# Kernel optimization log

Hardware: AMD Instinct MI355X
Metric: run time of the kernel (lower is better)

Reference implementation:

```python
import jax, jax.numpy as jnp
import numpy as np

# dims (match init_kwargs)
N, M = 128, 2048
DX, DY, DU, DZ = 64, 8, 256, 256
EPS = 0.01


def setup_inputs() -> dict:
    key = jax.random.key(0)
    kit = iter(jax.random.split(key, 40))
    def w(*shape):
        fan_in = shape[-1]
        return jax.random.normal(next(kit), shape, jnp.float32) / np.float32(np.sqrt(fan_in))
    def b(*shape):
        return 0.1 * jax.random.normal(next(kit), shape, jnp.float32)
    inp = {
        'X_tensor': jax.random.normal(next(kit), (N, DX), jnp.float32),
        'U_tensor': jax.random.normal(next(kit), (M, DY), jnp.float32),
        'Y_tensor': jax.random.normal(next(kit), (N, DY), jnp.float32),
        # context path (x -> u_i)
        'Wt0': w(DU, DX), 'bt0': b(DU),
        'Wt1': w(DU, DU), 'bt1': b(DU),
        # PICNN cell 0 (input cell, no z term)
        'Wyu0': w(DY, DX), 'byu0': b(DY), 'Wy0': w(DZ, DY), 'Wu0': w(DZ, DX), 'b0': b(DZ),
        # PICNN cell 1 (hidden cell, nonneg Wz1 via softplus)
        'Wzu1': w(DZ, DU), 'bzu1': b(DZ), 'Wz1': w(DZ, DZ),
        'Wyu1': w(DY, DU), 'byu1': b(DY), 'Wy1': w(DZ, DY), 'Wu1': w(DZ, DU), 'b1': b(DZ),
        # PICNN cell 2 (output cell, scalar potential)
        'Wzu2': w(DZ, DU), 'bzu2': b(DZ), 'Wz2': w(1, DZ),
        'Wyu2': w(DY, DU), 'byu2': b(DY), 'Wy2': w(1, DY), 'Wu2': w(1, DU), 'b2': b(1),
    }
    return inp


def _psi(X, U, Y, Wt0, bt0, Wt1, bt1, Wyu0, byu0, Wy0, Wu0, b0,
         Wzu1, bzu1, Wz1, Wyu1, byu1, Wy1, Wu1, b1,
         Wzu2, bzu2, Wz2, Wyu2, byu2, Wy2, Wu2, b2):
    relu = jax.nn.relu
    # context path depends only on X -> compute once per row, broadcast over m samples
    u1 = relu(X @ Wt0.T + bt0)                       # [n, du]
    u2 = relu(u1 @ Wt1.T + bt1)                      # [n, du]
    # cell 0: z1 [n, m, dz]  (pairwise over X rows x U samples)
    gy0 = X @ Wyu0.T + byu0                          # [n, dy]
    z1 = relu(jnp.einsum('md,nd,zd->nmz', U, gy0, Wy0)
              + (X @ Wu0.T + b0)[:, None, :])
    # cell 1: hidden convex cell with nonneg z-weight
    gz1 = relu(u1 @ Wzu1.T + bzu1)                   # [n, dz]
    gy1 = u1 @ Wyu1.T + byu1                         # [n, dy]
    z2 = relu(jnp.einsum('nmz,nz,kz->nmk', z1, gz1, jax.nn.softplus(Wz1))
              + jnp.einsum('md,nd,kd->nmk', U, gy1, Wy1)
              + (u1 @ Wu1.T + b1)[:, None, :])       # [n, m, dz]
    # output cell -> scalar potential phi(x_i, u_j)
    gz2 = relu(u2 @ Wzu2.T + bzu2)                   # [n, dz]
    gy2 = u2 @ Wyu2.T + byu2                         # [n, dy]
    phi = (jnp.einsum('nmz,nz,z->nm', z2, gz2, jax.nn.softplus(Wz2)[0])
           + jnp.einsum('md,nd,d->nm', U, gy2, Wy2[0])
           + (u2 @ Wu2[0] + b2[0])[:, None])         # [n, m]
    # entropic OT dual psi with stable row-wise logsumexp
    cost = Y @ U.T                                   # [n, m]
    slack = cost - phi
    row_max = jnp.max(slack, axis=1, keepdims=True)
    log_mean_exp = (jax.nn.logsumexp((slack - row_max) / EPS, axis=1, keepdims=True)
                    - jnp.log(jnp.float32(slack.shape[1])))
    return EPS * (log_mean_exp + row_max / EPS)      # [n, 1]


def reference(X_tensor, U_tensor, Y_tensor, Wt0, bt0, Wt1, bt1, Wyu0, byu0, Wy0, Wu0, b0,
              Wzu1, bzu1, Wz1, Wyu1, byu1, Wy1, Wu1, b1,
              Wzu2, bzu2, Wz2, Wyu2, byu2, Wy2, Wu2, b2):
    return _psi(X_tensor, U_tensor, Y_tensor, Wt0, bt0, Wt1, bt1, Wyu0, byu0, Wy0, Wu0, b0,
                Wzu1, bzu1, Wz1, Wyu1, byu1, Wy1, Wu1, b1,
                Wzu2, bzu2, Wz2, Wyu2, byu2, Wy2, Wu2, b2)
```

## Files before the change

kernel.cpp:

```cpp
#include <hip/hip_runtime.h>

#define NN 128
#define MM 2048
#define EPSF 0.01f

typedef __bf16 bf16x8 __attribute__((ext_vector_type(8)));
typedef __bf16 bf16x4 __attribute__((ext_vector_type(4)));
typedef float  f32x4  __attribute__((ext_vector_type(4)));

#define WS_SLACK 0
#define WS_W2    262144
#define WS_GZ1   294912
#define WS_YV    327680
#define WS_CU2   328704
#define WS_WTF   328832
#define WS_A2    361600
#define WS_B2    394368
#define WS_BX    918656
#define WS_U1    1442944
#define WS_U2    1459328
#define WS_C0    1475712
#define WS_C1    1492096
#define WS_GY0   1508480
#define WS_GY1   1509504

__device__ __forceinline__ float softplusf(float x) {
    return x > 20.f ? x : log1pf(expf(x));
}

__device__ __forceinline__ bf16x8 ld_cvt8(const float* __restrict__ p) {
    const float4* p4 = (const float4*)p;
    float4 a = p4[0], b = p4[1];
    bf16x8 r;
    r[0] = (__bf16)a.x; r[1] = (__bf16)a.y; r[2] = (__bf16)a.z; r[3] = (__bf16)a.w;
    r[4] = (__bf16)b.x; r[5] = (__bf16)b.y; r[6] = (__bf16)b.z; r[7] = (__bf16)b.w;
    return r;
}

__global__ __launch_bounds__(256) void k_l1(
    const float* __restrict__ X,
    const float* __restrict__ Wt0, const float* __restrict__ bt0,
    const float* __restrict__ Wu0, const float* __restrict__ b0,
    const float* __restrict__ Wyu0, const float* __restrict__ byu0,
    float* __restrict__ ws)
{
    const int t = threadIdx.x, w = t >> 6, lane = t & 63;
    const int c = lane & 15, q = lane >> 4;
    const int nb = blockIdx.y * 16;
    const int ct = blockIdx.x * 4 + w;
    if (ct >= 33) return;

    bf16x8 a1[2];
#pragma unroll
    for (int ch = 0; ch < 2; ++ch)
        a1[ch] = ld_cvt8(X + (nb + c) * 64 + ch * 32 + q * 8);

    const float* rp;
    int col;
    if (ct < 16)      { col = ct * 16 + c;        rp = Wt0 + col * 64; }
    else if (ct < 32) { col = (ct - 16) * 16 + c; rp = Wu0 + col * 64; }
    else              { col = c & 7;              rp = Wyu0 + col * 64; }

    f32x4 D = {0.f, 0.f, 0.f, 0.f};
#pragma unroll
    for (int ch = 0; ch < 2; ++ch) {
        bf16x8 b = ld_cvt8(rp + ch * 32 + q * 8);
        D = __builtin_amdgcn_mfma_f32_16x16x32_bf16(a1[ch], b, D, 0, 0, 0);
    }

    if (ct < 16) {
        __bf16* u1p = (__bf16*)(ws + WS_U1);
        const float bv = bt0[col];
#pragma unroll
        for (int r = 0; r < 4; ++r)
            u1p[(nb + 4 * q + r) * 256 + col] = (__bf16)fmaxf(D[r] + bv, 0.f);
    } else if (ct < 32) {
        __bf16* c0p = (__bf16*)(ws + WS_C0);
        const float bv = b0[col];
#pragma unroll
        for (int r = 0; r < 4; ++r)
            c0p[(nb + 4 * q + r) * 256 + col] = (__bf16)(D[r] + bv);
    } else if (c < 8) {
        const float bv = byu0[c];
#pragma unroll
        for (int r = 0; r < 4; ++r)
            ws[WS_GY0 + (nb + 4 * q + r) * 8 + c] = D[r] + bv;
    }
}

__global__ __launch_bounds__(256) void k_l2(
    const float* __restrict__ Wt1, const float* __restrict__ bt1,
    const float* __restrict__ Wzu1, const float* __restrict__ bzu1,
    const float* __restrict__ Wu1, const float* __restrict__ b1,
    const float* __restrict__ Wyu1, const float* __restrict__ byu1,
    float* __restrict__ ws)
{
    const int t = threadIdx.x, w = t >> 6, lane = t & 63;
    const int c = lane & 15, q = lane >> 4;
    const int nb = blockIdx.y * 16;
    const int ct = blockIdx.x * 4 + w;
    if (ct >= 49) return;

    const __bf16* u1p = (const __bf16*)(ws + WS_U1);
    bf16x8 aF[8];
#pragma unroll
    for (int ch = 0; ch < 8; ++ch)
        aF[ch] = *(const bf16x8*)(u1p + (nb + c) * 256 + ch * 32 + q * 8);

    const float* rp;
    int col;
    if (ct < 16)      { col = ct * 16 + c;        rp = Wt1 + col * 256; }
    else if (ct < 32) { col = (ct - 16) * 16 + c; rp = Wzu1 + col * 256; }
    else if (ct < 48) { col = (ct - 32) * 16 + c; rp = Wu1 + col * 256; }
    else              { col = c & 7;              rp = Wyu1 + col * 256; }

    f32x4 D = {0.f, 0.f, 0.f, 0.f};
#pragma unroll
    for (int ch = 0; ch < 8; ++ch) {
        bf16x8 b = ld_cvt8(rp + ch * 32 + q * 8);
        D = __builtin_amdgcn_mfma_f32_16x16x32_bf16(aF[ch], b, D, 0, 0, 0);
    }

    if (ct < 16) {
        __bf16* u2p = (__bf16*)(ws + WS_U2);
        const float bv = bt1[col];
#pragma unroll
        for (int r = 0; r < 4; ++r)
            u2p[(nb + 4 * q + r) * 256 + col] = (__bf16)fmaxf(D[r] + bv, 0.f);
    } else if (ct < 32) {
        const float bv = bzu1[col];
#pragma unroll
        for (int r = 0; r < 4; ++r)
            ws[WS_GZ1 + (nb + 4 * q + r) * 256 + col] = fmaxf(D[r] + bv, 0.f);
    } else if (ct < 48) {
        __bf16* c1p = (__bf16*)(ws + WS_C1);
        const float bv = b1[col];
#pragma unroll
        for (int r = 0; r < 4; ++r)
            c1p[(nb + 4 * q + r) * 256 + col] = (__bf16)(D[r] + bv);
    } else if (c < 8) {
        const float bv = byu1[c];
#pragma unroll
        for (int r = 0; r < 4; ++r)
            ws[WS_GY1 + (nb + 4 * q + r) * 8 + c] = D[r] + bv;
    }
}

__global__ __launch_bounds__(256) void k_l3(
    const float* __restrict__ Y,
    const float* __restrict__ Wzu2, const float* __restrict__ bzu2,
    const float* __restrict__ Wz2,
    const float* __restrict__ Wyu2, const float* __restrict__ byu2,
    const float* __restrict__ Wy2,
    const float* __restrict__ Wu2, const float* __restrict__ b2,
    float* __restrict__ ws)
{
    const int t = threadIdx.x, w = t >> 6, lane = t & 63;
    const int c = lane & 15, q = lane >> 4;
    const int nb = blockIdx.y * 16;
    const int ct = blockIdx.x * 4 + w;
    if (ct >= 17) return;

    const __bf16* u2p = (const __bf16*)(ws + WS_U2);
    bf16x8 aF[8];
#pragma unroll
    for (int ch = 0; ch < 8; ++ch)
        aF[ch] = *(const bf16x8*)(u2p + (nb + c) * 256 + ch * 32 + q * 8);

    const float* rp;
    int col = 0;
    if (ct < 16) { col = ct * 16 + c; rp = Wzu2 + col * 256; }
    else         { rp = (c < 8) ? (Wyu2 + c * 256) : Wu2; }

    f32x4 D = {0.f, 0.f, 0.f, 0.f};
#pragma unroll
    for (int ch = 0; ch < 8; ++ch) {
        bf16x8 b = ld_cvt8(rp + ch * 32 + q * 8);
        D = __builtin_amdgcn_mfma_f32_16x16x32_bf16(aF[ch], b, D, 0, 0, 0);
    }

    if (ct < 16) {
        const float bv = bzu2[col];
        const float sp = softplusf(Wz2[col]);
#pragma unroll
        for (int r = 0; r < 4; ++r) {
            float gz2 = fmaxf(D[r] + bv, 0.f);
            ws[WS_W2 + (nb + 4 * q + r) * 256 + col] = gz2 * sp;
        }
    } else if (c < 8) {
        const float bv = byu2[c];
        const float wy2 = Wy2[c];
#pragma unroll
        for (int r = 0; r < 4; ++r) {
            const int n = nb + 4 * q + r;
            ws[WS_YV + n * 8 + c] = Y[n * 8 + c] - (D[r] + bv) * wy2;
        }
    } else if (c == 8) {
#pragma unroll
        for (int r = 0; r < 4; ++r)
            ws[WS_CU2 + nb + 4 * q + r] = D[r] + b2[0];
    }
}

__global__ __launch_bounds__(256) void k_bmat(
    const float* __restrict__ Wz1, const float* __restrict__ U,
    const float* __restrict__ Wy0, const float* __restrict__ Wy1,
    float* __restrict__ ws)
{
    const int b = blockIdx.x, t = threadIdx.x;
    const int i = b * 256 + t;

    if (b < 64) {
        const int o = i * 4;
        const int j0 = o & 7;
        const int c  = (o >> 3) & 15;
        const int q  = (o >> 7) & 3;
        const int ch = (o >> 9) & 7;
        const int kt = o >> 12;
        const float* src = Wz1 + (kt * 16 + c) * 256 + ch * 32 + q * 8 + j0;
        float4 v = *(const float4*)src;
        bf16x4 r;
        r[0] = (__bf16)softplusf(v.x); r[1] = (__bf16)softplusf(v.y);
        r[2] = (__bf16)softplusf(v.z); r[3] = (__bf16)softplusf(v.w);
        *(bf16x4*)((__bf16*)(ws + WS_WTF) + o) = r;
    }
    {
        int m = i >> 5, cc = i & 31;
        float v = cc < 8 ? U[m * 8 + cc] : (cc == 8 ? 1.f : 0.f);
        ((__bf16*)(ws + WS_A2))[i] = (__bf16)v;
    }

    const int which = b >> 7, n = b & 127, z = t;
    const float* wy = (which ? Wy1 : Wy0) + z * 8;
    const float* gy = ws + (which ? WS_GY1 : WS_GY0) + n * 8;
    const __bf16* cp = (const __bf16*)(ws + (which ? WS_C1 : WS_C0)) + n * 256 + z;
    __bf16* dst = (__bf16*)(ws + (which ? WS_BX : WS_B2)) + (n * 256 + z) * 32;

    bf16x8 zz;
#pragma unroll
    for (int j = 0; j < 8; ++j) zz[j] = (__bf16)0.f;
    bf16x8 v0, v1 = zz;
#pragma unroll
    for (int d = 0; d < 8; ++d) v0[d] = (__bf16)(gy[d] * wy[d]);
    v1[0] = *cp;
    *(bf16x8*)(dst)      = v0;
    *(bf16x8*)(dst + 8)  = v1;
    *(bf16x8*)(dst + 16) = zz;
    *(bf16x8*)(dst + 24) = zz;
}

__global__ __launch_bounds__(256, 4) void k_main(
    const float* __restrict__ U,
    float* __restrict__ ws)
{
    __shared__ __bf16 zh[64][264];
    __shared__ float gz1s[256];
    __shared__ float w2s[256];
    __shared__ float sdot[64];
    __shared__ float psum[4][64];

    const int t  = threadIdx.x;
    const int n  = blockIdx.y;
    const int m0 = blockIdx.x * 64;
    const int w    = t >> 6;
    const int lane = t & 63;
    const int c = lane & 15;
    const int q = lane >> 4;

    gz1s[t] = ws[WS_GZ1 + n * 256 + t];
    w2s[t]  = ws[WS_W2  + n * 256 + t];
    if (t < 64) {
        float sd = 0.f;
#pragma unroll
        for (int d = 0; d < 8; ++d)
            sd += U[(m0 + t) * 8 + d] * ws[WS_YV + n * 8 + d];
        sdot[t] = sd;
    }

    const __bf16* A2p = (const __bf16*)(ws + WS_A2);
    const __bf16* B2p = (const __bf16*)(ws + WS_B2) + n * 8192;
    const __bf16* BXp = (const __bf16*)(ws + WS_BX) + n * 8192;
    const __bf16* WTF = (const __bf16*)(ws + WS_WTF);

    bf16x8 a2f[4];
#pragma unroll
    for (int mi = 0; mi < 4; ++mi)
        a2f[mi] = *(const bf16x8*)(A2p + (m0 + 16 * mi + c) * 32 + q * 8);

    {
        bf16x8 b2f[4];
#pragma unroll
        for (int zt = 0; zt < 4; ++zt)
            b2f[zt] = *(const bf16x8*)(B2p + (64 * w + 16 * zt + c) * 32 + q * 8);
        f32x4 pre[4][4];
#pragma unroll
        for (int zt = 0; zt < 4; ++zt)
#pragma unroll
            for (int mi = 0; mi < 4; ++mi) {
                f32x4 zacc = {0.f, 0.f, 0.f, 0.f};
                pre[zt][mi] = __builtin_amdgcn_mfma_f32_16x16x32_bf16(
                    b2f[zt], a2f[mi], zacc, 0, 0, 0);
            }
#pragma unroll
        for (int zt = 0; zt < 4; ++zt) {
            const int zb = 64 * w + 16 * zt + 4 * q;
#pragma unroll
            for (int mi = 0; mi < 4; ++mi) {
                bf16x4 v4;
#pragma unroll
                for (int r = 0; r < 4; ++r)
                    v4[r] = (__bf16)(fmaxf(pre[zt][mi][r], 0.f) * gz1s[zb + r]);
                *(bf16x4*)&zh[c + 16 * mi][zb] = v4;
            }
        }
    }

    f32x4 acc[4][4];
#pragma unroll
    for (int mi = 0; mi < 4; ++mi)
#pragma unroll
        for (int kj = 0; kj < 4; ++kj)
            acc[mi][kj] = f32x4{0.f, 0.f, 0.f, 0.f};

    __syncthreads();

    for (int ch = 0; ch < 8; ++ch) {
        bf16x8 az[4], bw[4];
#pragma unroll
        for (int mi = 0; mi < 4; ++mi)
            az[mi] = *(const bf16x8*)&zh[c + 16 * mi][ch * 32 + q * 8];
#pragma unroll
        for (int kj = 0; kj < 4; ++kj)
            bw[kj] = *(const bf16x8*)(WTF + ((4 * w + kj) * 8 + ch) * 512 + lane * 8);
#pragma unroll
        for (int mi = 0; mi < 4; ++mi)
#pragma unroll
            for (int kj = 0; kj < 4; ++kj)
                acc[mi][kj] = __builtin_amdgcn_mfma_f32_16x16x32_bf16(
                    az[mi], bw[kj], acc[mi][kj], 0, 0, 0);
    }
    {
        bf16x8 bx[4];
#pragma unroll
        for (int kj = 0; kj < 4; ++kj)
            bx[kj] = *(const bf16x8*)(BXp + (64 * w + 16 * kj + c) * 32 + q * 8);
#pragma unroll
        for (int mi = 0; mi < 4; ++mi)
#pragma unroll
            for (int kj = 0; kj < 4; ++kj)
                acc[mi][kj] = __builtin_amdgcn_mfma_f32_16x16x32_bf16(
                    a2f[mi], bx[kj], acc[mi][kj], 0, 0, 0);
    }

    float p[4][4];
#pragma unroll
    for (int mi = 0; mi < 4; ++mi)
#pragma unroll
        for (int r = 0; r < 4; ++r) p[mi][r] = 0.f;
#pragma unroll
    for (int kj = 0; kj < 4; ++kj) {
        float w2v = w2s[64 * w + 16 * kj + c];
#pragma unroll
        for (int mi = 0; mi < 4; ++mi)
#pragma unroll
            for (int r = 0; r < 4; ++r)
                p[mi][r] += fmaxf(acc[mi][kj][r], 0.f) * w2v;
    }
#pragma unroll
    for (int mi = 0; mi < 4; ++mi)
#pragma unroll
        for (int r = 0; r < 4; ++r) {
            float v = p[mi][r];
            v += __shfl_xor(v, 8);
            v += __shfl_xor(v, 4);
            v += __shfl_xor(v, 2);
            v += __shfl_xor(v, 1);
            p[mi][r] = v;
        }
    if (c == 0) {
#pragma unroll
        for (int mi = 0; mi < 4; ++mi)
            *(float4*)&psum[w][16 * mi + 4 * q] =
                make_float4(p[mi][0], p[mi][1], p[mi][2], p[mi][3]);
    }
    __syncthreads();
    if (t < 64) {
        float cu2 = ws[WS_CU2 + n];
        float pp = psum[0][t] + psum[1][t] + psum[2][t] + psum[3][t];
        ws[WS_SLACK + n * 2048 + m0 + t] = sdot[t] - cu2 - pp;
    }
}

__global__ __launch_bounds__(256) void k_lse(const float* __restrict__ ws,
                                             float* __restrict__ out) {
    __shared__ float redmax[4];
    __shared__ float redsum[4];
    const int n = blockIdx.x;
    const int t = threadIdx.x;
    const float* s = ws + WS_SLACK + n * 2048;

    float vals[8];
    float mx = -3.4e38f;
#pragma unroll
    for (int i = 0; i < 8; ++i) {
        vals[i] = s[t + 256 * i];
        mx = fmaxf(mx, vals[i]);
    }
#pragma unroll
    for (int off = 32; off; off >>= 1) mx = fmaxf(mx, __shfl_xor(mx, off));
    if ((t & 63) == 0) redmax[t >> 6] = mx;
    __syncthreads();
    mx = fmaxf(fmaxf(redmax[0], redmax[1]), fmaxf(redmax[2], redmax[3]));

    float sum = 0.f;
#pragma unroll
    for (int i = 0; i < 8; ++i) sum += expf((vals[i] - mx) * (1.f / EPSF));
#pragma unroll
    for (int off = 32; off; off >>= 1) sum += __shfl_xor(sum, off);
    if ((t & 63) == 0) redsum[t >> 6] = sum;
    __syncthreads();
    if (t == 0) {
        float S = redsum[0] + redsum[1] + redsum[2] + redsum[3];
        out[n] = EPSF * logf(S * (1.f / 2048.f)) + mx;
    }
}

extern "C" void kernel_launch(void* const* d_in, const int* in_sizes, int n_in,
                              void* d_out, int out_size, void* d_ws, size_t ws_size,
                              hipStream_t stream) {
    const float* X    = (const float*)d_in[0];
    const float* Uu   = (const float*)d_in[1];
    const float* Yy   = (const float*)d_in[2];
    const float* Wt0  = (const float*)d_in[3];
    const float* bt0  = (const float*)d_in[4];
    const float* Wt1  = (const float*)d_in[5];
    const float* bt1  = (const float*)d_in[6];
    const float* Wyu0 = (const float*)d_in[7];
    const float* byu0 = (const float*)d_in[8];
    const float* Wy0  = (const float*)d_in[9];
    const float* Wu0  = (const float*)d_in[10];
    const float* b0   = (const float*)d_in[11];
    const float* Wzu1 = (const float*)d_in[12];
    const float* bzu1 = (const float*)d_in[13];
    const float* Wz1  = (const float*)d_in[14];
    const float* Wyu1 = (const float*)d_in[15];
    const float* byu1 = (const float*)d_in[16];
    const float* Wy1  = (const float*)d_in[17];
    const float* Wu1  = (const float*)d_in[18];
    const float* b1   = (const float*)d_in[19];
    const float* Wzu2 = (const float*)d_in[20];
    const float* bzu2 = (const float*)d_in[21];
    const float* Wz2  = (const float*)d_in[22];
    const float* Wyu2 = (const float*)d_in[23];
    const float* byu2 = (const float*)d_in[24];
    const float* Wy2  = (const float*)d_in[25];
    const float* Wu2  = (const float*)d_in[26];
    const float* b2   = (const float*)d_in[27];
    float* ws  = (float*)d_ws;
    float* out = (float*)d_out;

    k_l1<<<dim3(9, 8),  dim3(256), 0, stream>>>(X, Wt0, bt0, Wu0, b0, Wyu0, byu0, ws);
    k_l2<<<dim3(13, 8), dim3(256), 0, stream>>>(Wt1, bt1, Wzu1, bzu1, Wu1, b1, Wyu1, byu1, ws);
    k_l3<<<dim3(5, 8),  dim3(256), 0, stream>>>(Yy, Wzu2, bzu2, Wz2, Wyu2, byu2, Wy2, Wu2, b2, ws);
    k_bmat<<<dim3(256), dim3(256), 0, stream>>>(Wz1, Uu, Wy0, Wy1, ws);
    k_main<<<dim3(MM / 64, NN), dim3(256), 0, stream>>>(Uu, ws);
    k_lse<<<dim3(128), dim3(256), 0, stream>>>(ws, out);
}
```

Measured before the change: 175.3 us.

## Fuse prologue kernels with grid barriers and fold logsumexp into main kernel

Merges the three context-layer kernels and the B-matrix packing kernel into one persistent 256-block kernel that separates dependent stages with atomic-counter grid barriers. The logsumexp kernel is removed: the last k_main block to finish each row, detected with a per-row atomic counter, does the row reduction. This is meant to cut launch overhead and inter-kernel gaps from six launches to two plus a memset. In exchange it relies on all 256 blocks being co-resident for the spin barrier, and it reuses the barrier word at ws[0] (slack row 0) and the U1 region as counters, which adds correctness risk.

```diff
diff --git a/kernel.cpp b/kernel.cpp
--- a/kernel.cpp
+++ b/kernel.cpp
@@ -37,117 +37,30 @@
     return r;
 }
 
-__global__ __launch_bounds__(256) void k_l1(
-    const float* __restrict__ X,
+__device__ __forceinline__ void gbar(unsigned* cnt, unsigned target) {
+    __syncthreads();
+    if (threadIdx.x == 0) {
+        __threadfence();
+        atomicAdd(cnt, 1u);
+        while (atomicAdd(cnt, 0u) < target) __builtin_amdgcn_s_sleep(2);
+        __threadfence();
+    }
+    __syncthreads();
+}
+
+__global__ __launch_bounds__(256) void k_ctx2(
+    const float* __restrict__ X, const float* __restrict__ Y,
+    const float* __restrict__ U,
     const float* __restrict__ Wt0, const float* __restrict__ bt0,
+    const float* __restrict__ Wt1, const float* __restrict__ bt1,
+    const float* __restrict__ Wyu0, const float* __restrict__ byu0,
+    const float* __restrict__ Wy0,
     const float* __restrict__ Wu0, const float* __restrict__ b0,
-    const float* __restrict__ Wyu0, const float* __restrict__ byu0,
-    float* __restrict__ ws)
-{
-    const int t = threadIdx.x, w = t >> 6, lane = t & 63;
-    const int c = lane & 15, q = lane >> 4;
-    const int nb = blockIdx.y * 16;
-    const int ct = blockIdx.x * 4 + w;
-    if (ct >= 33) return;
-
-    bf16x8 a1[2];
-#pragma unroll
-    for (int ch = 0; ch < 2; ++ch)
-        a1[ch] = ld_cvt8(X + (nb + c) * 64 + ch * 32 + q * 8);
-
-    const float* rp;
-    int col;
-    if (ct < 16)      { col = ct * 16 + c;        rp = Wt0 + col * 64; }
-    else if (ct < 32) { col = (ct - 16) * 16 + c; rp = Wu0 + col * 64; }
-    else              { col = c & 7;              rp = Wyu0 + col * 64; }
-
-    f32x4 D = {0.f, 0.f, 0.f, 0.f};
-#pragma unroll
-    for (int ch = 0; ch < 2; ++ch) {
-        bf16x8 b = ld_cvt8(rp + ch * 32 + q * 8);
-        D = __builtin_amdgcn_mfma_f32_16x16x32_bf16(a1[ch], b, D, 0, 0, 0);
-    }
-
-    if (ct < 16) {
-        __bf16* u1p = (__bf16*)(ws + WS_U1);
-        const float bv = bt0[col];
-#pragma unroll
-        for (int r = 0; r < 4; ++r)
-            u1p[(nb + 4 * q + r) * 256 + col] = (__bf16)fmaxf(D[r] + bv, 0.f);
-    } else if (ct < 32) {
-        __bf16* c0p = (__bf16*)(ws + WS_C0);
-        const float bv = b0[col];
-#pragma unroll
-        for (int r = 0; r < 4; ++r)
-            c0p[(nb + 4 * q + r) * 256 + col] = (__bf16)(D[r] + bv);
-    } else if (c < 8) {
-        const float bv = byu0[c];
-#pragma unroll
-        for (int r = 0; r < 4; ++r)
-            ws[WS_GY0 + (nb + 4 * q + r) * 8 + c] = D[r] + bv;
-    }
-}
-
-__global__ __launch_bounds__(256) void k_l2(
-    const float* __restrict__ Wt1, const float* __restrict__ bt1,
     const float* __restrict__ Wzu1, const float* __restrict__ bzu1,
+    const float* __restrict__ Wz1,
+    const float* __restrict__ Wyu1, const float* __restrict__ byu1,
+    const float* __restrict__ Wy1,
     const float* __restrict__ Wu1, const float* __restrict__ b1,
-    const float* __restrict__ Wyu1, const float* __restrict__ byu1,
-    float* __restrict__ ws)
-{
-    const int t = threadIdx.x, w = t >> 6, lane = t & 63;
-    const int c = lane & 15, q = lane >> 4;
-    const int nb = blockIdx.y * 16;
-    const int ct = blockIdx.x * 4 + w;
-    if (ct >= 49) return;
-
-    const __bf16* u1p = (const __bf16*)(ws + WS_U1);
-    bf16x8 aF[8];
-#pragma unroll
-    for (int ch = 0; ch < 8; ++ch)
-        aF[ch] = *(const bf16x8*)(u1p + (nb + c) * 256 + ch * 32 + q * 8);
-
-    const float* rp;
-    int col;
-    if (ct < 16)      { col = ct * 16 + c;        rp = Wt1 + col * 256; }
-    else if (ct < 32) { col = (ct - 16) * 16 + c; rp = Wzu1 + col * 256; }
-    else if (ct < 48) { col = (ct - 32) * 16 + c; rp = Wu1 + col * 256; }
-    else              { col = c & 7;              rp = Wyu1 + col * 256; }
-
-    f32x4 D = {0.f, 0.f, 0.f, 0.f};
-#pragma unroll
-    for (int ch = 0; ch < 8; ++ch) {
-        bf16x8 b = ld_cvt8(rp + ch * 32 + q * 8);
-        D = __builtin_amdgcn_mfma_f32_16x16x32_bf16(aF[ch], b, D, 0, 0, 0);
-    }
-
-    if (ct < 16) {
-        __bf16* u2p = (__bf16*)(ws + WS_U2);
-        const float bv = bt1[col];
-#pragma unroll
-        for (int r = 0; r < 4; ++r)
-            u2p[(nb + 4 * q + r) * 256 + col] = (__bf16)fmaxf(D[r] + bv, 0.f);
-    } else if (ct < 32) {
-        const float bv = bzu1[col];
-#pragma unroll
-        for (int r = 0; r < 4; ++r)
-            ws[WS_GZ1 + (nb + 4 * q + r) * 256 + col] = fmaxf(D[r] + bv, 0.f);
-    } else if (ct < 48) {
-        __bf16* c1p = (__bf16*)(ws + WS_C1);
-        const float bv = b1[col];
-#pragma unroll
-        for (int r = 0; r < 4; ++r)
-            c1p[(nb + 4 * q + r) * 256 + col] = (__bf16)(D[r] + bv);
-    } else if (c < 8) {
-        const float bv = byu1[c];
-#pragma unroll
-        for (int r = 0; r < 4; ++r)
-            ws[WS_GY1 + (nb + 4 * q + r) * 8 + c] = D[r] + bv;
-    }
-}
-
-__global__ __launch_bounds__(256) void k_l3(
-    const float* __restrict__ Y,
     const float* __restrict__ Wzu2, const float* __restrict__ bzu2,
     const float* __restrict__ Wz2,
     const float* __restrict__ Wyu2, const float* __restrict__ byu2,
@@ -155,69 +68,57 @@
     const float* __restrict__ Wu2, const float* __restrict__ b2,
     float* __restrict__ ws)
 {
-    const int t = threadIdx.x, w = t >> 6, lane = t & 63;
+    const int t = threadIdx.x, b = blockIdx.x;
+    const int w = t >> 6, lane = t & 63;
     const int c = lane & 15, q = lane >> 4;
-    const int nb = blockIdx.y * 16;
-    const int ct = blockIdx.x * 4 + w;
-    if (ct >= 17) return;
-
-    const __bf16* u2p = (const __bf16*)(ws + WS_U2);
-    bf16x8 aF[8];
-#pragma unroll
-    for (int ch = 0; ch < 8; ++ch)
-        aF[ch] = *(const bf16x8*)(u2p + (nb + c) * 256 + ch * 32 + q * 8);
-
-    const float* rp;
-    int col = 0;
-    if (ct < 16) { col = ct * 16 + c; rp = Wzu2 + col * 256; }
-    else         { rp = (c < 8) ? (Wyu2 + c * 256) : Wu2; }
-
-    f32x4 D = {0.f, 0.f, 0.f, 0.f};
-#pragma unroll
-    for (int ch = 0; ch < 8; ++ch) {
-        bf16x8 b = ld_cvt8(rp + ch * 32 + q * 8);
-        D = __builtin_amdgcn_mfma_f32_16x16x32_bf16(aF[ch], b, D, 0, 0, 0);
-    }
-
-    if (ct < 16) {
-        const float bv = bzu2[col];
-        const float sp = softplusf(Wz2[col]);
-#pragma unroll
-        for (int r = 0; r < 4; ++r) {
-            float gz2 = fmaxf(D[r] + bv, 0.f);
-            ws[WS_W2 + (nb + 4 * q + r) * 256 + col] = gz2 * sp;
-        }
-    } else if (c < 8) {
-        const float bv = byu2[c];
-        const float wy2 = Wy2[c];
-#pragma unroll
-        for (int r = 0; r < 4; ++r) {
-            const int n = nb + 4 * q + r;
-            ws[WS_YV + n * 8 + c] = Y[n * 8 + c] - (D[r] + bv) * wy2;
-        }
-    } else if (c == 8) {
-#pragma unroll
-        for (int r = 0; r < 4; ++r)
-            ws[WS_CU2 + nb + 4 * q + r] = D[r] + b2[0];
-    }
-}
-
-__global__ __launch_bounds__(256) void k_bmat(
-    const float* __restrict__ Wz1, const float* __restrict__ U,
-    const float* __restrict__ Wy0, const float* __restrict__ Wy1,
-    float* __restrict__ ws)
-{
-    const int b = blockIdx.x, t = threadIdx.x;
-    const int i = b * 256 + t;
-
+    const int g = b * 4 + w;
+    unsigned* bar = (unsigned*)ws;
+
+    if (g < 264) {
+        const int nb = (g / 33) * 16;
+        const int ct = g % 33;
+        bf16x8 a1[2];
+#pragma unroll
+        for (int ch = 0; ch < 2; ++ch)
+            a1[ch] = ld_cvt8(X + (nb + c) * 64 + ch * 32 + q * 8);
+        const float* rp;
+        int col;
+        if (ct < 16)      { col = ct * 16 + c;        rp = Wt0 + col * 64; }
+        else if (ct < 32) { col = (ct - 16) * 16 + c; rp = Wu0 + col * 64; }
+        else              { col = c & 7;              rp = Wyu0 + col * 64; }
+        f32x4 D = {0.f, 0.f, 0.f, 0.f};
+#pragma unroll
+        for (int ch = 0; ch < 2; ++ch) {
+            bf16x8 bb = ld_cvt8(rp + ch * 32 + q * 8);
+            D = __builtin_amdgcn_mfma_f32_16x16x32_bf16(a1[ch], bb, D, 0, 0, 0);
+        }
+        if (ct < 16) {
+            __bf16* u1p = (__bf16*)(ws + WS_U1);
+            const float bv = bt0[col];
+#pragma unroll
+            for (int r = 0; r < 4; ++r)
+                u1p[(nb + 4 * q + r) * 256 + col] = (__bf16)fmaxf(D[r] + bv, 0.f);
+        } else if (ct < 32) {
+            __bf16* c0p = (__bf16*)(ws + WS_C0);
+            const float bv = b0[col];
+#pragma unroll
+            for (int r = 0; r < 4; ++r)
+                c0p[(nb + 4 * q + r) * 256 + col] = (__bf16)(D[r] + bv);
+        } else if (c < 8) {
+            const float bv = byu0[c];
+#pragma unroll
+            for (int r = 0; r < 4; ++r)
+                ws[WS_GY0 + (nb + 4 * q + r) * 8 + c] = D[r] + bv;
+        }
+    }
     if (b < 64) {
-        const int o = i * 4;
+        const int o = (b * 256 + t) * 4;
         const int j0 = o & 7;
-        const int c  = (o >> 3) & 15;
-        const int q  = (o >> 7) & 3;
+        const int cc = (o >> 3) & 15;
+        const int qq = (o >> 7) & 3;
         const int ch = (o >> 9) & 7;
         const int kt = o >> 12;
-        const float* src = Wz1 + (kt * 16 + c) * 256 + ch * 32 + q * 8 + j0;
+        const float* src = Wz1 + (kt * 16 + cc) * 256 + ch * 32 + qq * 8 + j0;
         float4 v = *(const float4*)src;
         bf16x4 r;
         r[0] = (__bf16)softplusf(v.x); r[1] = (__bf16)softplusf(v.y);
@@ -225,39 +126,150 @@
         *(bf16x4*)((__bf16*)(ws + WS_WTF) + o) = r;
     }
     {
-        int m = i >> 5, cc = i & 31;
+        const int i = b * 256 + t;
+        const int m = i >> 5, cc = i & 31;
         float v = cc < 8 ? U[m * 8 + cc] : (cc == 8 ? 1.f : 0.f);
         ((__bf16*)(ws + WS_A2))[i] = (__bf16)v;
     }
-
-    const int which = b >> 7, n = b & 127, z = t;
-    const float* wy = (which ? Wy1 : Wy0) + z * 8;
-    const float* gy = ws + (which ? WS_GY1 : WS_GY0) + n * 8;
-    const __bf16* cp = (const __bf16*)(ws + (which ? WS_C1 : WS_C0)) + n * 256 + z;
-    __bf16* dst = (__bf16*)(ws + (which ? WS_BX : WS_B2)) + (n * 256 + z) * 32;
-
-    bf16x8 zz;
-#pragma unroll
-    for (int j = 0; j < 8; ++j) zz[j] = (__bf16)0.f;
-    bf16x8 v0, v1 = zz;
-#pragma unroll
-    for (int d = 0; d < 8; ++d) v0[d] = (__bf16)(gy[d] * wy[d]);
-    v1[0] = *cp;
-    *(bf16x8*)(dst)      = v0;
-    *(bf16x8*)(dst + 8)  = v1;
-    *(bf16x8*)(dst + 16) = zz;
-    *(bf16x8*)(dst + 24) = zz;
+    gbar(bar, 256u);
+
+    if (g < 392) {
+        const int nb = (g / 49) * 16;
+        const int ct = g % 49;
+        const __bf16* u1p = (const __bf16*)(ws + WS_U1);
+        bf16x8 aF[8];
+#pragma unroll
+        for (int ch = 0; ch < 8; ++ch)
+            aF[ch] = *(const bf16x8*)(u1p + (nb + c) * 256 + ch * 32 + q * 8);
+        const float* rp;
+        int col;
+        if (ct < 16)      { col = ct * 16 + c;        rp = Wt1 + col * 256; }
+        else if (ct < 32) { col = (ct - 16) * 16 + c; rp = Wzu1 + col * 256; }
+        else if (ct < 48) { col = (ct - 32) * 16 + c; rp = Wu1 + col * 256; }
+        else              { col = c & 7;              rp = Wyu1 + col * 256; }
+        f32x4 D = {0.f, 0.f, 0.f, 0.f};
+#pragma unroll
+        for (int ch = 0; ch < 8; ++ch) {
+            bf16x8 bb = ld_cvt8(rp + ch * 32 + q * 8);
+            D = __builtin_amdgcn_mfma_f32_16x16x32_bf16(aF[ch], bb, D, 0, 0, 0);
+        }
+        if (ct < 16) {
+            __bf16* u2p = (__bf16*)(ws + WS_U2);
+            const float bv = bt1[col];
+#pragma unroll
+            for (int r = 0; r < 4; ++r)
+                u2p[(nb + 4 * q + r) * 256 + col] = (__bf16)fmaxf(D[r] + bv, 0.f);
+        } else if (ct < 32) {
+            const float bv = bzu1[col];
+#pragma unroll
+            for (int r = 0; r < 4; ++r)
+                ws[WS_GZ1 + (nb + 4 * q + r) * 256 + col] = fmaxf(D[r] + bv, 0.f);
+        } else if (ct < 48) {
+            __bf16* c1p = (__bf16*)(ws + WS_C1);
+            const float bv = b1[col];
+#pragma unroll
+            for (int r = 0; r < 4; ++r)
+                c1p[(nb + 4 * q + r) * 256 + col] = (__bf16)(D[r] + bv);
+        } else if (c < 8) {
+            const float bv = byu1[c];
+#pragma unroll
+            for (int r = 0; r < 4; ++r)
+                ws[WS_GY1 + (nb + 4 * q + r) * 8 + c] = D[r] + bv;
+        }
+    }
+    if (b < 128) {
+        const int n = b, z = t;
+        const float* wy = Wy0 + z * 8;
+        const float* gy = ws + WS_GY0 + n * 8;
+        const __bf16* cp = (const __bf16*)(ws + WS_C0) + n * 256 + z;
+        __bf16* dst = (__bf16*)(ws + WS_B2) + (n * 256 + z) * 32;
+        bf16x8 zz;
+#pragma unroll
+        for (int j = 0; j < 8; ++j) zz[j] = (__bf16)0.f;
+        bf16x8 v0, v1 = zz;
+#pragma unroll
+        for (int d = 0; d < 8; ++d) v0[d] = (__bf16)(gy[d] * wy[d]);
+        v1[0] = *cp;
+        *(bf16x8*)(dst)      = v0;
+        *(bf16x8*)(dst + 8)  = v1;
+        *(bf16x8*)(dst + 16) = zz;
+        *(bf16x8*)(dst + 24) = zz;
+    }
+    gbar(bar, 512u);
+
+    if (g < 136) {
+        const int nb = (g / 17) * 16;
+        const int ct = g % 17;
+        const __bf16* u2p = (const __bf16*)(ws + WS_U2);
+        bf16x8 aF[8];
+#pragma unroll
+        for (int ch = 0; ch < 8; ++ch)
+            aF[ch] = *(const bf16x8*)(u2p + (nb + c) * 256 + ch * 32 + q * 8);
+        const float* rp;
+        int col = 0;
+        if (ct < 16) { col = ct * 16 + c; rp = Wzu2 + col * 256; }
+        else         { rp = (c < 8) ? (Wyu2 + c * 256) : Wu2; }
+        f32x4 D = {0.f, 0.f, 0.f, 0.f};
+#pragma unroll
+        for (int ch = 0; ch < 8; ++ch) {
+            bf16x8 bb = ld_cvt8(rp + ch * 32 + q * 8);
+            D = __builtin_amdgcn_mfma_f32_16x16x32_bf16(aF[ch], bb, D, 0, 0, 0);
+        }
+        if (ct < 16) {
+            const float bv = bzu2[col];
+            const float sp = softplusf(Wz2[col]);
+#pragma unroll
+            for (int r = 0; r < 4; ++r) {
+                float gz2 = fmaxf(D[r] + bv, 0.f);
+                ws[WS_W2 + (nb + 4 * q + r) * 256 + col] = gz2 * sp;
+            }
+        } else if (c < 8) {
+            const float bv = byu2[c];
+            const float wy2 = Wy2[c];
+#pragma unroll
+            for (int r = 0; r < 4; ++r) {
+                const int n = nb + 4 * q + r;
+                ws[WS_YV + n * 8 + c] = Y[n * 8 + c] - (D[r] + bv) * wy2;
+            }
+        } else if (c == 8) {
+#pragma unroll
+            for (int r = 0; r < 4; ++r)
+                ws[WS_CU2 + nb + 4 * q + r] = D[r] + b2[0];
+        }
+    }
+    if (b >= 128) {
+        const int n = b - 128, z = t;
+        const float* wy = Wy1 + z * 8;
+        const float* gy = ws + WS_GY1 + n * 8;
+        const __bf16* cp = (const __bf16*)(ws + WS_C1) + n * 256 + z;
+        __bf16* dst = (__bf16*)(ws + WS_BX) + (n * 256 + z) * 32;
+        bf16x8 zz;
+#pragma unroll
+        for (int j = 0; j < 8; ++j) zz[j] = (__bf16)0.f;
+        bf16x8 v0, v1 = zz;
+#pragma unroll
+        for (int d = 0; d < 8; ++d) v0[d] = (__bf16)(gy[d] * wy[d]);
+        v1[0] = *cp;
+        *(bf16x8*)(dst)      = v0;
+        *(bf16x8*)(dst + 8)  = v1;
+        *(bf16x8*)(dst + 16) = zz;
+        *(bf16x8*)(dst + 24) = zz;
+    }
+    if (b == 0 && t < 128) ((unsigned*)(ws + WS_U1))[t] = 0u;
 }
 
 __global__ __launch_bounds__(256, 4) void k_main(
     const float* __restrict__ U,
-    float* __restrict__ ws)
+    float* __restrict__ ws,
+    float* __restrict__ out)
 {
     __shared__ __bf16 zh[64][264];
     __shared__ float gz1s[256];
     __shared__ float w2s[256];
     __shared__ float sdot[64];
     __shared__ float psum[4][64];
+    __shared__ float redsh[8];
+    __shared__ int lastf;
 
     const int t  = threadIdx.x;
     const int n  = blockIdx.y;
@@ -389,39 +401,42 @@
         float pp = psum[0][t] + psum[1][t] + psum[2][t] + psum[3][t];
         ws[WS_SLACK + n * 2048 + m0 + t] = sdot[t] - cu2 - pp;
     }
-}
-
-__global__ __launch_bounds__(256) void k_lse(const float* __restrict__ ws,
-                                             float* __restrict__ out) {
-    __shared__ float redmax[4];
-    __shared__ float redsum[4];
-    const int n = blockIdx.x;
-    const int t = threadIdx.x;
-    const float* s = ws + WS_SLACK + n * 2048;
-
-    float vals[8];
-    float mx = -3.4e38f;
-#pragma unroll
-    for (int i = 0; i < 8; ++i) {
-        vals[i] = s[t + 256 * i];
-        mx = fmaxf(mx, vals[i]);
-    }
-#pragma unroll
-    for (int off = 32; off; off >>= 1) mx = fmaxf(mx, __shfl_xor(mx, off));
-    if ((t & 63) == 0) redmax[t >> 6] = mx;
-    __syncthreads();
-    mx = fmaxf(fmaxf(redmax[0], redmax[1]), fmaxf(redmax[2], redmax[3]));
-
-    float sum = 0.f;
-#pragma unroll
-    for (int i = 0; i < 8; ++i) sum += expf((vals[i] - mx) * (1.f / EPSF));
-#pragma unroll
-    for (int off = 32; off; off >>= 1) sum += __shfl_xor(sum, off);
-    if ((t & 63) == 0) redsum[t >> 6] = sum;
+
+    __threadfence();
     __syncthreads();
     if (t == 0) {
-        float S = redsum[0] + redsum[1] + redsum[2] + redsum[3];
-        out[n] = EPSF * logf(S * (1.f / 2048.f)) + mx;
+        unsigned* lcnt = (unsigned*)(ws + WS_U1);
+        unsigned old = atomicAdd(lcnt + n, 1u);
+        lastf = (old == 31u) ? 1 : 0;
+    }
+    __syncthreads();
+    if (lastf) {
+        __threadfence();
+        const float* s = ws + WS_SLACK + n * 2048;
+        float vals[8];
+        float mx = -3.4e38f;
+#pragma unroll
+        for (int i = 0; i < 8; ++i) {
+            vals[i] = s[t + 256 * i];
+            mx = fmaxf(mx, vals[i]);
+        }
+#pragma unroll
+        for (int off = 32; off; off >>= 1) mx = fmaxf(mx, __shfl_xor(mx, off));
+        if ((t & 63) == 0) redsh[t >> 6] = mx;
+        __syncthreads();
+        mx = fmaxf(fmaxf(redsh[0], redsh[1]), fmaxf(redsh[2], redsh[3]));
+
+        float sum = 0.f;
+#pragma unroll
+        for (int i = 0; i < 8; ++i) sum += expf((vals[i] - mx) * (1.f / EPSF));
+#pragma unroll
+        for (int off = 32; off; off >>= 1) sum += __shfl_xor(sum, off);
+        if ((t & 63) == 0) redsh[4 + (t >> 6)] = sum;
+        __syncthreads();
+        if (t == 0) {
+            float S = redsh[4] + redsh[5] + redsh[6] + redsh[7];
+            out[n] = EPSF * logf(S * (1.f / 2048.f)) + mx;
+        }
     }
 }
 
@@ -459,10 +474,10 @@
     float* ws  = (float*)d_ws;
     float* out = (float*)d_out;
 
-    k_l1<<<dim3(9, 8),  dim3(256), 0, stream>>>(X, Wt0, bt0, Wu0, b0, Wyu0, byu0, ws);
-    k_l2<<<dim3(13, 8), dim3(256), 0, stream>>>(Wt1, bt1, Wzu1, bzu1, Wu1, b1, Wyu1, byu1, ws);
-    k_l3<<<dim3(5, 8),  dim3(256), 0, stream>>>(Yy, Wzu2, bzu2, Wz2, Wyu2, byu2, Wy2, Wu2, b2, ws);
-    k_bmat<<<dim3(256), dim3(256), 0, stream>>>(Wz1, Uu, Wy0, Wy1, ws);
-    k_main<<<dim3(MM / 64, NN), dim3(256), 0, stream>>>(Uu, ws);
-    k_lse<<<dim3(128), dim3(256), 0, stream>>>(ws, out);
-}
+    hipMemsetAsync(ws, 0, 4, stream);
+    k_ctx2<<<dim3(256), dim3(256), 0, stream>>>(
+        X, Yy, Uu, Wt0, bt0, Wt1, bt1, Wyu0, byu0, Wy0, Wu0, b0,
+        Wzu1, bzu1, Wz1, Wyu1, byu1, Wy1, Wu1, b1,
+        Wzu2, bzu2, Wz2, Wyu2, byu2, Wy2, Wu2, b2, ws);
+    k_main<<<dim3(MM / 64, NN), dim3(256), 0, stream>>>(Uu, ws, out);
+}
```

After: 585.2 us. 3.34x slower.
